# Kernel tuning notes

Measured on AMD Instinct MI355X. Metric: run time of the kernel, lower is better.

Reference implementation:

```python
import jax, jax.numpy as jnp
import numpy as np

B, S, E, H = 4, 2048, 1024, 16
D = E // H  # key_size


def setup_inputs() -> dict:
    key = jax.random.key(0)
    ks = jax.random.split(key, 6)
    s = 1.0 / np.sqrt(E)
    return {
        "X": jax.random.normal(ks[0], (B, S, E), dtype=jnp.float32),
        "Wq": jax.random.uniform(ks[1], (E, E), jnp.float32, -s, s),
        "Wk": jax.random.uniform(ks[2], (E, E), jnp.float32, -s, s),
        "Wv": jax.random.uniform(ks[3], (E, E), jnp.float32, -s, s),
        "Wo": jax.random.uniform(ks[4], (E, E), jnp.float32, -s, s),
        "bo": jax.random.uniform(ks[5], (E,), jnp.float32, -s, s),
    }


def reference(X, Wq, Wk, Wv, Wo, bo):
    # Linear layers: y = x @ W^T (torch convention), no bias for q/k/v
    def split(x):  # [B,S,E] -> [B,H,S,D]
        return x.reshape(B, S, H, D).transpose(0, 2, 1, 3)

    q = split(X @ Wq.T)
    k = split(X @ Wk.T)
    v = split(X @ Wv.T)
    scale = jnp.asarray(np.sqrt(D), dtype=X.dtype)
    scores = jnp.einsum("bhqd,bhkd->bhqk", q, k) / scale
    probs = jax.nn.softmax(scores, axis=-1)
    ctx = jnp.einsum("bhqk,bhkd->bhqd", probs, v)
    out = ctx.transpose(0, 2, 1, 3).reshape(B, S, E)
    return out @ Wo.T + bo
```

## Files before the change

kernel.cpp:

```cpp
#include <hip/hip_runtime.h>
#include <hip/hip_bf16.h>

typedef short bf16x8 __attribute__((ext_vector_type(8)));
typedef float f32x4  __attribute__((ext_vector_type(4)));

__device__ __forceinline__ short f2bf(float f) {
    union { float f; unsigned u; } x; x.f = f;
    unsigned r = x.u + 0x7fffu + ((x.u >> 16) & 1u);
    return (short)(r >> 16);
}

__device__ __forceinline__ unsigned rbits(float f) {
    union { float f; unsigned u; } x; x.f = f;
    return x.u + 0x8000u;
}
__device__ __forceinline__ int pack2(float a, float b) {
    return (int)__builtin_amdgcn_perm(rbits(b), rbits(a), 0x07060302u);
}

__device__ __forceinline__ f32x4 mfma32k(bf16x8 a, bf16x8 b, f32x4 c) {
    return __builtin_amdgcn_mfma_f32_16x16x32_bf16(a, b, c, 0, 0, 0);
}

#define GLDS16(g, l)                                                            \
    __builtin_amdgcn_global_load_lds(                                           \
        (const __attribute__((address_space(1))) void*)(g),                     \
        (__attribute__((address_space(3))) void*)(l), 16, 0, 0)

static constexpr int Bb = 4, Ss = 2048, Ee = 1024, Hh = 16, Dd = 64;
static constexpr int Mrows = Bb * Ss;
static constexpr float CL2 = 0.1803368801111204f;

__global__ void cvt_all(const float* __restrict__ X,  const float* __restrict__ Wq,
                        const float* __restrict__ Wk, const float* __restrict__ Wv,
                        const float* __restrict__ Wo,
                        short* __restrict__ Xb, short* __restrict__ Wqk,
                        short* __restrict__ Wvb, short* __restrict__ Wob) {
    int bid = blockIdx.x;
    const float* src; short* dst; int off; float scale = 1.0f;
    if (bid < 8192) {
        src = X; dst = Xb; off = bid * 1024;
    } else {
        int wsel = (bid - 8192) >> 10;
        off = ((bid - 8192) & 1023) * 1024;
        if      (wsel == 0) { src = Wq; dst = Wqk;                scale = CL2; }
        else if (wsel == 1) { src = Wk; dst = Wqk + Ee * Ee; }
        else if (wsel == 2) { src = Wv; dst = Wvb; }
        else                { src = Wo; dst = Wob; }
    }
    int i = off + threadIdx.x * 4;
    float4 v = *(const float4*)(src + i);
    short4 o;
    o.x = f2bf(v.x * scale); o.y = f2bf(v.y * scale);
    o.z = f2bf(v.z * scale); o.w = f2bf(v.w * scale);
    *(short4*)(dst + i) = o;
}

template<bool BIAS_F32OUT, bool PERMC>
__global__ __launch_bounds__(256, 2)
void gemm_bt(const short* __restrict__ A, int lda,
             const short* __restrict__ Bm, int ldb,
             void* __restrict__ C, int ldc,
             const float* __restrict__ bias, int K) {
    __shared__ __align__(16) short sA[2 * 128 * 32];
    __shared__ __align__(16) short sB[2 * 128 * 32];
    const int t = threadIdx.x, w = t >> 6, l = t & 63;
    const int lane16 = l & 15, quad = l >> 4;
    const int wm = (w >> 1) * 64, wn = (w & 1) * 64;
    const int bm = blockIdx.x, bn = blockIdx.y;

    f32x4 acc[4][4] = {};
    const short* Ab = A + (size_t)bm * 128 * lda;
    const short* Bbp = Bm + (size_t)bn * 128 * ldb;

    for (int k0 = 0; k0 < K; k0 += 64) {
#pragma unroll
        for (int p = 0; p < 4; ++p) {
            int c = p * 256 + t;
            int panel = c >> 9, row = (c >> 2) & 127, cs = c & 3;
            int col = k0 + panel * 32 + cs * 8;
            short* ldst = (p * 256 + w * 64) * 8 + (short*)nullptr;
            GLDS16(Ab + (size_t)row * lda + col, sA + (p * 256 + w * 64) * 8);
            GLDS16(Bbp + (size_t)row * ldb + col, sB + (p * 256 + w * 64) * 8);
            (void)ldst;
        }
        __syncthreads();
#pragma unroll
        for (int s2 = 0; s2 < 2; ++s2) {
            bf16x8 af[4], bfr[4];
#pragma unroll
            for (int i = 0; i < 4; ++i) {
                af[i]  = *(const bf16x8*)(sA + s2 * 4096 + (wm + i * 16 + lane16) * 32 + quad * 8);
                bfr[i] = *(const bf16x8*)(sB + s2 * 4096 + (wn + i * 16 + lane16) * 32 + quad * 8);
            }
#pragma unroll
            for (int i = 0; i < 4; ++i)
#pragma unroll
                for (int j = 0; j < 4; ++j)
                    acc[i][j] = mfma32k(af[i], bfr[j], acc[i][j]);
        }
        __syncthreads();
    }

    const int sEven = (lane16 >> 2) * 8 + (lane16 & 3);
#pragma unroll
    for (int i = 0; i < 4; ++i)
#pragma unroll
        for (int j = 0; j < 4; ++j) {
            int row = bm * 128 + wm + i * 16 + quad * 4;
            int col = bn * 128 + wn + j * 16 + lane16;
            if (BIAS_F32OUT) {
                float bv = bias[col];
                float* Cf = (float*)C;
#pragma unroll
                for (int r = 0; r < 4; ++r)
                    Cf[(size_t)(row + r) * ldc + col] = acc[i][j][r] + bv;
            } else {
                if (PERMC) col = (col & ~31) | (sEven + (j & 1) * 4);
                short* Cb = (short*)C;
#pragma unroll
                for (int r = 0; r < 4; ++r)
                    Cb[(size_t)(row + r) * ldc + col] = f2bf(acc[i][j][r]);
            }
        }
}

__global__ __launch_bounds__(256, 4)
void attn_kernel(const short* __restrict__ QK, const short* __restrict__ VT,
                 short* __restrict__ CTX) {
    __shared__ __align__(16) short sK[8192];
    __shared__ __align__(16) short sV[8192];
    const int t = threadIdx.x, w = t >> 6, l = t & 63;
    const int lane16 = l & 15, quad = l >> 4;
    const int bh = blockIdx.x, qt = blockIdx.y;
    const int b = bh >> 4, h = bh & 15;

    const short* Qb = QK + ((size_t)(b * 2048 + qt * 128)) * 2048 + h * 64;
    const short* Kb = QK + ((size_t)(b * 2048)) * 2048 + 1024 + h * 64;
    const short* Vb = VT + ((size_t)(h * 64)) * 8192 + (size_t)b * 2048;

#pragma unroll
    for (int p = 0; p < 4; ++p) {
        int c = p * 256 + t;
        int half = c >> 9, row = (c >> 2) & 127, dq = c & 3;
        GLDS16(Qb + (size_t)row * 2048 + half * 32 + dq * 8, sK + (p * 256 + w * 64) * 8);
    }
    __syncthreads();
    bf16x8 qf[2][2];
#pragma unroll
    for (int mt = 0; mt < 2; ++mt)
#pragma unroll
        for (int ks = 0; ks < 2; ++ks)
            qf[mt][ks] = *(const bf16x8*)(sK + ks * 4096 + (w * 32 + mt * 16 + lane16) * 32 + quad * 8);
    __syncthreads();

    f32x4 l4[2] = {};
    f32x4 o[2][4] = {};

    for (int kt = 0; kt < 16; ++kt) {
        const short* KbT = Kb + (size_t)kt * 128 * 2048;
        const short* VbT = Vb + kt * 128;
#pragma unroll
        for (int p = 0; p < 4; ++p) {
            int c = p * 256 + t;
            int half = c >> 9, row = (c >> 2) & 127, dq = c & 3;
            GLDS16(KbT + (size_t)row * 2048 + half * 32 + dq * 8, sK + (p * 256 + w * 64) * 8);
        }
#pragma unroll
        for (int p = 0; p < 4; ++p) {
            int c = p * 256 + t;
            int kb = c >> 8, d = (c >> 2) & 63, kq = c & 3;
            GLDS16(VbT + (size_t)d * 8192 + kb * 32 + kq * 8, sV + (p * 256 + w * 64) * 8);
        }
        __syncthreads();

#pragma unroll
        for (int a = 0; a < 4; ++a) {
            f32x4 sc[2][2] = {};
#pragma unroll
            for (int sub = 0; sub < 2; ++sub) {
                int nt = a * 2 + sub;
                bf16x8 kf0 = *(const bf16x8*)(sK + (nt * 16 + lane16) * 32 + quad * 8);
                bf16x8 kf1 = *(const bf16x8*)(sK + 4096 + (nt * 16 + lane16) * 32 + quad * 8);
#pragma unroll
                for (int mt = 0; mt < 2; ++mt) {
                    sc[mt][sub] = mfma32k(kf0, qf[mt][0], sc[mt][sub]);
                    sc[mt][sub] = mfma32k(kf1, qf[mt][1], sc[mt][sub]);
                }
            }
            bf16x8 pf[2];
#pragma unroll
            for (int mt = 0; mt < 2; ++mt) {
                union { int i[4]; bf16x8 v; } u;
#pragma unroll
                for (int sub = 0; sub < 2; ++sub) {
                    f32x4 e;
#pragma unroll
                    for (int r = 0; r < 4; ++r)
                        e[r] = __builtin_amdgcn_exp2f(sc[mt][sub][r]);
                    l4[mt] += e;
                    u.i[sub * 2]     = pack2(e[0], e[1]);
                    u.i[sub * 2 + 1] = pack2(e[2], e[3]);
                }
                pf[mt] = u.v;
            }
#pragma unroll
            for (int dt = 0; dt < 4; ++dt) {
                bf16x8 vf = *(const bf16x8*)(sV + a * 2048 + (dt * 16 + lane16) * 32 + quad * 8);
#pragma unroll
                for (int mt = 0; mt < 2; ++mt)
                    o[mt][dt] = mfma32k(pf[mt], vf, o[mt][dt]);
            }
        }
        __syncthreads();
    }

    float l_i[2];
#pragma unroll
    for (int mt = 0; mt < 2; ++mt) {
        l_i[mt] = (l4[mt][0] + l4[mt][1]) + (l4[mt][2] + l4[mt][3]);
        l_i[mt] += __shfl_xor(l_i[mt], 16);
        l_i[mt] += __shfl_xor(l_i[mt], 32);
    }
#pragma unroll
    for (int mt = 0; mt < 2; ++mt)
#pragma unroll
        for (int r = 0; r < 4; ++r) {
            float lr = __shfl(l_i[mt], quad * 4 + r);
            float inv = 1.0f / lr;
            int row = b * 2048 + qt * 128 + w * 32 + mt * 16 + quad * 4 + r;
#pragma unroll
            for (int dt = 0; dt < 4; ++dt)
                CTX[(size_t)row * 1024 + h * 64 + dt * 16 + lane16] = f2bf(o[mt][dt][r] * inv);
        }
}

extern "C" void kernel_launch(void* const* d_in, const int* in_sizes, int n_in,
                              void* d_out, int out_size, void* d_ws, size_t ws_size,
                              hipStream_t stream) {
    const float* X  = (const float*)d_in[0];
    const float* Wq = (const float*)d_in[1];
    const float* Wk = (const float*)d_in[2];
    const float* Wv = (const float*)d_in[3];
    const float* Wo = (const float*)d_in[4];
    const float* bo = (const float*)d_in[5];
    float* out = (float*)d_out;

    char* ws = (char*)d_ws;
    constexpr size_t OFF_XB  = 0;
    constexpr size_t OFF_WQK = OFF_XB  + (size_t)Mrows * Ee * 2;
    constexpr size_t OFF_WV  = OFF_WQK + (size_t)2 * Ee * Ee * 2;
    constexpr size_t OFF_WO  = OFF_WV  + (size_t)Ee * Ee * 2;
    constexpr size_t OFF_QK  = OFF_WO  + (size_t)Ee * Ee * 2;
    constexpr size_t OFF_VT  = OFF_QK  + (size_t)Mrows * 2048 * 2;
    constexpr size_t OFF_CTX = OFF_VT  + (size_t)Ee * Mrows * 2;
    short* Xb   = (short*)(ws + OFF_XB);
    short* Wqk  = (short*)(ws + OFF_WQK);
    short* Wvb  = (short*)(ws + OFF_WV);
    short* Wob  = (short*)(ws + OFF_WO);
    short* QKb  = (short*)(ws + OFF_QK);
    short* VTb  = (short*)(ws + OFF_VT);
    short* CTX  = (short*)(ws + OFF_CTX);

    cvt_all<<<12288, 256, 0, stream>>>(X, Wq, Wk, Wv, Wo, Xb, Wqk, Wvb, Wob);

    gemm_bt<false, false><<<dim3(Mrows / 128, 2048 / 128), 256, 0, stream>>>(
        Xb, Ee, Wqk, Ee, QKb, 2048, nullptr, Ee);

    gemm_bt<false, true><<<dim3(Ee / 128, Mrows / 128), 256, 0, stream>>>(
        Wvb, Ee, Xb, Ee, VTb, Mrows, nullptr, Ee);

    attn_kernel<<<dim3(Bb * Hh, Ss / 128), 256, 0, stream>>>(QKb, VTb, CTX);

    gemm_bt<true, false><<<dim3(Mrows / 128, Ee / 128), 256, 0, stream>>>(
        CTX, Ee, Wob, Ee, out, Ee, bo, Ee);
}
```

Before: 275.1 us.

## Double-buffer LDS tiles in GEMM and attention kernels to overlap loads with MFMA

The GEMM now walks K in 32-wide steps with two LDS buffers. It prefetches the next step's A/B tiles into the idle buffer while MFMAs consume the current one, leaving one barrier per iteration. The attention kernel double-buffers its K/V tiles the same way: it preloads the first tile, then prefetches tile kt+1 while computing on tile kt. The goal is to hide global-to-LDS latency behind compute. In exchange, attention LDS use doubles and its launch bound drops from 4 to 2 blocks per CU, which lowers occupancy, and the GEMM runs twice as many barrier iterations.

```diff
diff --git a/kernel.cpp b/kernel.cpp
--- a/kernel.cpp
+++ b/kernel.cpp
@@ -72,34 +72,44 @@
     f32x4 acc[4][4] = {};
     const short* Ab = A + (size_t)bm * 128 * lda;
     const short* Bbp = Bm + (size_t)bn * 128 * ldb;
-
-    for (int k0 = 0; k0 < K; k0 += 64) {
-#pragma unroll
-        for (int p = 0; p < 4; ++p) {
-            int c = p * 256 + t;
-            int panel = c >> 9, row = (c >> 2) & 127, cs = c & 3;
-            int col = k0 + panel * 32 + cs * 8;
-            short* ldst = (p * 256 + w * 64) * 8 + (short*)nullptr;
-            GLDS16(Ab + (size_t)row * lda + col, sA + (p * 256 + w * 64) * 8);
-            GLDS16(Bbp + (size_t)row * ldb + col, sB + (p * 256 + w * 64) * 8);
-            (void)ldst;
-        }
+    const int s0 = w * 64 + l;
+    const int ldsOff = (w * 64) * 8;
+
+#pragma unroll
+    for (int p = 0; p < 2; ++p) {
+        int s = p * 256 + s0;
+        int row = s >> 2, cs = s & 3;
+        GLDS16(Ab + (size_t)row * lda + cs * 8, sA + p * 2048 + ldsOff);
+        GLDS16(Bbp + (size_t)row * ldb + cs * 8, sB + p * 2048 + ldsOff);
+    }
+
+    const int nIter = K >> 5;
+    for (int i = 0; i < nIter; ++i) {
         __syncthreads();
-#pragma unroll
-        for (int s2 = 0; s2 < 2; ++s2) {
-            bf16x8 af[4], bfr[4];
-#pragma unroll
-            for (int i = 0; i < 4; ++i) {
-                af[i]  = *(const bf16x8*)(sA + s2 * 4096 + (wm + i * 16 + lane16) * 32 + quad * 8);
-                bfr[i] = *(const bf16x8*)(sB + s2 * 4096 + (wn + i * 16 + lane16) * 32 + quad * 8);
-            }
-#pragma unroll
-            for (int i = 0; i < 4; ++i)
-#pragma unroll
-                for (int j = 0; j < 4; ++j)
-                    acc[i][j] = mfma32k(af[i], bfr[j], acc[i][j]);
-        }
-        __syncthreads();
+        if (i + 1 < nIter) {
+            int k0 = (i + 1) << 5;
+            int boff = ((i + 1) & 1) * 4096;
+#pragma unroll
+            for (int p = 0; p < 2; ++p) {
+                int s = p * 256 + s0;
+                int row = s >> 2, cs = s & 3;
+                GLDS16(Ab + (size_t)row * lda + k0 + cs * 8, sA + boff + p * 2048 + ldsOff);
+                GLDS16(Bbp + (size_t)row * ldb + k0 + cs * 8, sB + boff + p * 2048 + ldsOff);
+            }
+        }
+        const short* pA = sA + (i & 1) * 4096;
+        const short* pB = sB + (i & 1) * 4096;
+        bf16x8 af[4], bfr[4];
+#pragma unroll
+        for (int ii = 0; ii < 4; ++ii) {
+            af[ii]  = *(const bf16x8*)(pA + (wm + ii * 16 + lane16) * 32 + quad * 8);
+            bfr[ii] = *(const bf16x8*)(pB + (wn + ii * 16 + lane16) * 32 + quad * 8);
+        }
+#pragma unroll
+        for (int ii = 0; ii < 4; ++ii)
+#pragma unroll
+            for (int j = 0; j < 4; ++j)
+                acc[ii][j] = mfma32k(af[ii], bfr[j], acc[ii][j]);
     }
 
     const int sEven = (lane16 >> 2) * 8 + (lane16 & 3);
@@ -125,11 +135,11 @@
         }
 }
 
-__global__ __launch_bounds__(256, 4)
+__global__ __launch_bounds__(256, 2)
 void attn_kernel(const short* __restrict__ QK, const short* __restrict__ VT,
                  short* __restrict__ CTX) {
-    __shared__ __align__(16) short sK[8192];
-    __shared__ __align__(16) short sV[8192];
+    __shared__ __align__(16) short sKd[2 * 8192];
+    __shared__ __align__(16) short sVd[2 * 8192];
     const int t = threadIdx.x, w = t >> 6, l = t & 63;
     const int lane16 = l & 15, quad = l >> 4;
     const int bh = blockIdx.x, qt = blockIdx.y;
@@ -138,12 +148,14 @@
     const short* Qb = QK + ((size_t)(b * 2048 + qt * 128)) * 2048 + h * 64;
     const short* Kb = QK + ((size_t)(b * 2048)) * 2048 + 1024 + h * 64;
     const short* Vb = VT + ((size_t)(h * 64)) * 8192 + (size_t)b * 2048;
+    const int ldsOff = (w * 64) * 8;
+
 
 #pragma unroll
     for (int p = 0; p < 4; ++p) {
         int c = p * 256 + t;
         int half = c >> 9, row = (c >> 2) & 127, dq = c & 3;
-        GLDS16(Qb + (size_t)row * 2048 + half * 32 + dq * 8, sK + (p * 256 + w * 64) * 8);
+        GLDS16(Qb + (size_t)row * 2048 + half * 32 + dq * 8, sKd + p * 2048 + ldsOff);
     }
     __syncthreads();
     bf16x8 qf[2][2];
@@ -151,28 +163,48 @@
     for (int mt = 0; mt < 2; ++mt)
 #pragma unroll
         for (int ks = 0; ks < 2; ++ks)
-            qf[mt][ks] = *(const bf16x8*)(sK + ks * 4096 + (w * 32 + mt * 16 + lane16) * 32 + quad * 8);
+            qf[mt][ks] = *(const bf16x8*)(sKd + ks * 4096 + (w * 32 + mt * 16 + lane16) * 32 + quad * 8);
     __syncthreads();
+
+#pragma unroll
+    for (int p = 0; p < 4; ++p) {
+        int c = p * 256 + t;
+        int half = c >> 9, row = (c >> 2) & 127, dq = c & 3;
+        GLDS16(Kb + (size_t)row * 2048 + half * 32 + dq * 8, sKd + p * 2048 + ldsOff);
+    }
+#pragma unroll
+    for (int p = 0; p < 4; ++p) {
+        int c = p * 256 + t;
+        int kb = c >> 8, d = (c >> 2) & 63, kq = c & 3;
+        GLDS16(Vb + (size_t)d * 8192 + kb * 32 + kq * 8, sVd + p * 2048 + ldsOff);
+    }
 
     f32x4 l4[2] = {};
     f32x4 o[2][4] = {};
 
     for (int kt = 0; kt < 16; ++kt) {
-        const short* KbT = Kb + (size_t)kt * 128 * 2048;
-        const short* VbT = Vb + kt * 128;
-#pragma unroll
-        for (int p = 0; p < 4; ++p) {
-            int c = p * 256 + t;
-            int half = c >> 9, row = (c >> 2) & 127, dq = c & 3;
-            GLDS16(KbT + (size_t)row * 2048 + half * 32 + dq * 8, sK + (p * 256 + w * 64) * 8);
-        }
-#pragma unroll
-        for (int p = 0; p < 4; ++p) {
-            int c = p * 256 + t;
-            int kb = c >> 8, d = (c >> 2) & 63, kq = c & 3;
-            GLDS16(VbT + (size_t)d * 8192 + kb * 32 + kq * 8, sV + (p * 256 + w * 64) * 8);
-        }
         __syncthreads();
+        if (kt < 15) {
+            const short* KbT = Kb + (size_t)(kt + 1) * 128 * 2048;
+            const short* VbT = Vb + (kt + 1) * 128;
+            int boff = ((kt + 1) & 1) * 8192;
+#pragma unroll
+            for (int p = 0; p < 4; ++p) {
+                int c = p * 256 + t;
+                int half = c >> 9, row = (c >> 2) & 127, dq = c & 3;
+                GLDS16(KbT + (size_t)row * 2048 + half * 32 + dq * 8,
+                       sKd + boff + p * 2048 + ldsOff);
+            }
+#pragma unroll
+            for (int p = 0; p < 4; ++p) {
+                int c = p * 256 + t;
+                int kb = c >> 8, d = (c >> 2) & 63, kq = c & 3;
+                GLDS16(VbT + (size_t)d * 8192 + kb * 32 + kq * 8,
+                       sVd + boff + p * 2048 + ldsOff);
+            }
+        }
+        const short* sK = sKd + (kt & 1) * 8192;
+        const short* sV = sVd + (kt & 1) * 8192;
 
 #pragma unroll
         for (int a = 0; a < 4; ++a) {
@@ -212,7 +244,6 @@
                     o[mt][dt] = mfma32k(pf[mt], vf, o[mt][dt]);
             }
         }
-        __syncthreads();
     }
 
     float l_i[2];
```

After: 269.9 us. About the same (-1.9%).
